# Kernel tuning notes

Hardware: AMD Instinct MI355X
Metric: run time of the kernel (lower is better)

## Reference

```python
import jax, jax.numpy as jnp
import numpy as np

LAYERS = 2
HEADS = 4
TYPE_IDX = 1  # type='logic' -> 1
HIDDEN = 256
HEAD_DIM = HIDDEN // HEADS
EPS = 1e-6


def setup_inputs() -> dict:
    key = jax.random.key(0)
    ks = jax.random.split(key, 12)
    B, S, H = 4, 2048, HIDDEN
    inputs = jax.random.normal(ks[0], (B, S, H), jnp.float32)
    graphs = jax.random.uniform(ks[1], (B, 2, S, S), jnp.float32)
    biases_batch = jax.random.normal(ks[2], (B, 2, S, S), jnp.float32)
    s_h = 1.0 / np.sqrt(H).astype(np.float32)
    s_d = 1.0 / np.sqrt(HEAD_DIM).astype(np.float32)
    gc_w = jax.random.normal(ks[3], (LAYERS, H, H), jnp.float32) * s_h
    gc_b = jnp.zeros((LAYERS, H), jnp.float32)
    attn_w = jax.random.normal(ks[4], (LAYERS, HEAD_DIM, H), jnp.float32) * s_h  # conv1 (1x1) weight
    attn_a = jax.random.normal(ks[5], (LAYERS, HEAD_DIM), jnp.float32) * s_d     # conv2_1 (1x1) weight
    ln_a = jnp.ones((H,), jnp.float32)
    ln_b = jnp.zeros((H,), jnp.float32)
    w1 = jax.random.normal(ks[6], (H, H), jnp.float32) * s_h
    w1b = jnp.zeros((H,), jnp.float32)
    w2 = jax.random.normal(ks[7], (H, H), jnp.float32) * s_h
    w2b = jnp.zeros((H,), jnp.float32)
    return dict(inputs=inputs, graphs=graphs, biases_batch=biases_batch,
                gc_w=gc_w, gc_b=gc_b, attn_w=attn_w, attn_a=attn_a,
                ln_a=ln_a, ln_b=ln_b, w1=w1, w1b=w1b, w2=w2, w2b=w2b)


def reference(inputs, graphs, biases_batch, gc_w, gc_b, attn_w, attn_a, ln_a, ln_b, w1, w1b, w2, w2b):
    adj = graphs[:, TYPE_IDX]          # [b,s,s]
    bias = biases_batch[:, TYPE_IDX]   # [b,s,s]
    x0 = inputs
    x = inputs
    for i in range(LAYERS):
        # GraphConvolution: adj @ (x @ W) + b
        mf = jnp.einsum('bij,bjh->bih', adj, x @ gc_w[i]) + gc_b[i]
        # Node_Attn_head (NOTE: original uses conv2_1 for BOTH f_1 and f_2)
        seq_fts = jnp.einsum('bsh,dh->bsd', mf, attn_w[i])      # [b,s,d]
        f = seq_fts @ attn_a[i]                                  # [b,s]
        logits = jax.nn.leaky_relu(f[:, :, None] + f[:, None, :])  # f_2^T + f_1 -> [b,s,s]
        coefs = jax.nn.softmax(logits + bias, axis=1)            # Softmax(dim=1)
        ret = jax.nn.leaky_relu(jnp.einsum('bij,bjd->bid', coefs, seq_fts))  # [b,s,d]
        # shared attention head across all HEADS -> identical outputs, concatenated
        x = jnp.tile(ret, (1, 1, HEADS)) + x
    # LayerNorm (torch.std is unbiased -> ddof=1), residual to original inputs
    mean = x.mean(-1, keepdims=True)
    std = jnp.std(x, axis=-1, keepdims=True, ddof=1)
    g = ln_a * (x - mean) / (std + EPS) + ln_b + x0
    # PositionwiseFeedForward (dropout inactive in eval)
    ff = jax.nn.relu(g @ w1.T + w1b) @ w2.T + w2b
    return ff + g
```

## Files before the change

kernel.cpp:

```cpp
#include <hip/hip_runtime.h>
#include <math.h>

#define BB 4
#define SS 2048
#define HH 256
#define DD 64
#define NLAYERS 2
#define NPART 128

#define XSC  (1.f/64.f)
#define XSCI 64.f
#define FSC  (1.f/256.f)
#define WSC  256.f
#define LNWSC 5.5451774444795624f

typedef _Float16 f16;
typedef f16 half8 __attribute__((ext_vector_type(8)));
typedef f16 half4 __attribute__((ext_vector_type(4)));
typedef float f32x4 __attribute__((ext_vector_type(4)));
#define MFMA16(a, b, c) __builtin_amdgcn_mfma_f32_16x16x32_f16(a, b, c, 0, 0, 0)

__device__ __forceinline__ float lrelu(float v) { return v > 0.f ? v : 0.01f * v; }
__device__ __forceinline__ int enc(float f) { int i = __float_as_int(f); return i >= 0 ? i : (i ^ 0x7fffffff); }
__device__ __forceinline__ float dec(int k) { int i = k >= 0 ? k : (k ^ 0x7fffffff); return __int_as_float(i); }
__device__ __forceinline__ void split8(const float* v, half8& h, half8& l) {
    #pragma unroll
    for (int e = 0; e < 8; ++e) {
        f16 hh = (f16)v[e]; h[e] = hh; l[e] = (f16)((v[e] - (float)hh) * 2048.f);
    }
}

__global__ __launch_bounds__(256) void split_scale(
    const float* __restrict__ src, f16* __restrict__ dh, f16* __restrict__ dl, float scale)
{
    long i = ((long)blockIdx.x * 256 + threadIdx.x) * 8;
    float4 a = *(const float4*)&src[i];
    float4 b = *(const float4*)&src[i + 4];
    float v[8] = {a.x * scale, a.y * scale, a.z * scale, a.w * scale,
                  b.x * scale, b.y * scale, b.z * scale, b.w * scale};
    half8 h, l; split8(v, h, l);
    *(half8*)&dh[i] = h; *(half8*)&dl[i] = l;
}

__global__ __launch_bounds__(256) void prep_wy(
    const float* __restrict__ gc_w, const float* __restrict__ gc_b,
    const float* __restrict__ attn_w,
    f16* __restrict__ WysH, f16* __restrict__ WysL, float* __restrict__ by,
    const float* __restrict__ w1, const float* __restrict__ w2,
    f16* __restrict__ w1h, f16* __restrict__ w1l,
    f16* __restrict__ w2h, f16* __restrict__ w2l, int* __restrict__ FMXi)
{
    int L = blockIdx.x >> 6, d = blockIdx.x & 63;
    int h = threadIdx.x;
    const float* gwr = gc_w + (long)L * HH * HH + (long)h * HH;
    const float* aw = attn_w + (long)L * DD * HH + (long)d * HH;
    float acc = 0.f;
    #pragma unroll 4
    for (int hp = 0; hp < HH; hp += 4) {
        float4 g4 = *(const float4*)&gwr[hp];
        float4 a4 = *(const float4*)&aw[hp];
        acc += g4.x * a4.x + g4.y * a4.y + g4.z * a4.z + g4.w * a4.w;
    }
    f16 hh = (f16)acc;
    WysH[((long)L * DD + d) * HH + h] = hh;
    WysL[((long)L * DD + d) * HH + h] = (f16)((acc - (float)hh) * 2048.f);
    if (h == 0) {
        float ba = 0.f;
        const float* gb = gc_b + (long)L * HH;
        for (int hp = 0; hp < HH; ++hp) ba += gb[hp] * aw[hp];
        by[L * DD + d] = ba;
    }
    int gt = blockIdx.x * 256 + h;
    #pragma unroll
    for (int p = 0; p < 4; ++p) {
        int e = gt * 4 + p;
        if (e < 65536) {
            float v = w1[e]; f16 x = (f16)v;
            w1h[e] = x; w1l[e] = (f16)((v - (float)x) * 2048.f);
        } else {
            int e2 = e - 65536;
            float v = w2[e2]; f16 x = (f16)v;
            w2h[e2] = x; w2l[e2] = (f16)((v - (float)x) * 2048.f);
        }
    }
    if (blockIdx.x == 0 && h < 2 * BB) FMXi[h] = enc(-1e30f);
}

__global__ __launch_bounds__(256) void y_mfma(
    const f16* __restrict__ xh, const f16* __restrict__ xl,
    const f16* __restrict__ WyhL, const f16* __restrict__ WylL,
    f16* __restrict__ yTh, f16* __restrict__ yTl)
{
    const int tid = threadIdx.x;
    const int w = tid >> 6, l = tid & 63;
    const int gw = blockIdx.x * 4 + w;
    const int b = gw >> 7, st = gw & 127;
    const int s0 = st * 16;
    const int lr = l & 15, kg = (l >> 4) * 8;
    const f16* Aph = xh + ((long)b * SS + s0 + lr) * HH;
    const f16* Apl = xl + ((long)b * SS + s0 + lr) * HH;
    f32x4 acch[4] = {}, accm[4] = {};
    #pragma unroll
    for (int k0 = 0; k0 < HH; k0 += 32) {
        half8 ah = *(const half8*)(Aph + k0 + kg);
        half8 al = *(const half8*)(Apl + k0 + kg);
        #pragma unroll
        for (int dt = 0; dt < 4; ++dt) {
            long boff = (long)(dt * 16 + lr) * HH + k0 + kg;
            half8 bh = *(const half8*)(WyhL + boff);
            half8 bl = *(const half8*)(WylL + boff);
            acch[dt] = MFMA16(ah, bh, acch[dt]);
            accm[dt] = MFMA16(ah, bl, accm[dt]);
            accm[dt] = MFMA16(al, bh, accm[dt]);
        }
    }
    const int rg0 = (l >> 4) * 4;
    #pragma unroll
    for (int dt = 0; dt < 4; ++dt) {
        int d = dt * 16 + lr;
        half4 h4, l4;
        #pragma unroll
        for (int rr = 0; rr < 4; ++rr) {
            float v = acch[dt][rr] + accm[dt][rr] * (1.f / 2048.f);
            f16 hh = (f16)v; h4[rr] = hh; l4[rr] = (f16)((v - (float)hh) * 2048.f);
        }
        long ob = ((long)b * DD + d) * SS + s0 + rg0;
        *(half4*)(yTh + ob) = h4;
        *(half4*)(yTl + ob) = l4;
    }
}

__global__ __launch_bounds__(512, 2) void ftp_fused(
    const float* __restrict__ adjB,
    const f16* __restrict__ yTh, const f16* __restrict__ yTl,
    const float* __restrict__ byL, const float* __restrict__ aaL,
    float* __restrict__ F, f16* __restrict__ fTh, f16* __restrict__ fTl,
    int* __restrict__ fmxSlot)
{
    __shared__ float Ls[8][16][68];
    __shared__ float fmaxS[16];
    const int b = blockIdx.y;
    const int i0 = blockIdx.x * 16;
    const int tid = threadIdx.x;
    const int w = tid >> 6, l = tid & 63, lr = l & 15, kg = (l >> 4) * 8;
    const float* Arow = adjB + (long)b * 2 * SS * SS + (long)(i0 + lr) * SS;
    const f16* Bh = yTh + ((long)b * DD + lr) * SS;
    const f16* Bl = yTl + ((long)b * DD + lr) * SS;

    f32x4 acch[4] = {}, accm[4] = {};
    #pragma unroll
    for (int ks = 0; ks < 256; ks += 32) {
        int k = w * 256 + ks + kg;
        float4 a0 = *(const float4*)(Arow + k);
        float4 a1 = *(const float4*)(Arow + k + 4);
        float av[8] = {a0.x, a0.y, a0.z, a0.w, a1.x, a1.y, a1.z, a1.w};
        half8 ah, al; split8(av, ah, al);
        #pragma unroll
        for (int dt = 0; dt < 4; ++dt) {
            long off = (long)dt * 16 * SS + k;
            half8 bh = *(const half8*)(Bh + off);
            half8 bl = *(const half8*)(Bl + off);
            acch[dt] = MFMA16(ah, bh, acch[dt]);
            accm[dt] = MFMA16(ah, bl, accm[dt]);
            accm[dt] = MFMA16(al, bh, accm[dt]);
        }
    }
    const int rg0 = (l >> 4) * 4;
    #pragma unroll
    for (int dt = 0; dt < 4; ++dt)
        #pragma unroll
        for (int rr = 0; rr < 4; ++rr)
            Ls[w][rg0 + rr][dt * 16 + lr] = acch[dt][rr] + accm[dt][rr] * (1.f / 2048.f);
    __syncthreads();

    {
        int r = tid >> 5, q = tid & 31, c0 = q * 2;
        float s0 = 0.f, s1 = 0.f;
        #pragma unroll
        for (int ww = 0; ww < 8; ++ww) { s0 += Ls[ww][r][c0]; s1 += Ls[ww][r][c0 + 1]; }
        s0 = s0 * XSCI + byL[c0];
        s1 = s1 * XSCI + byL[c0 + 1];
        Ls[0][r][c0] = s0; Ls[0][r][c0 + 1] = s1;
        float dot = s0 * aaL[c0] + s1 * aaL[c0 + 1];
        dot += __shfl_xor(dot, 1, 64);
        dot += __shfl_xor(dot, 2, 64);
        dot += __shfl_xor(dot, 4, 64);
        dot += __shfl_xor(dot, 8, 64);
        dot += __shfl_xor(dot, 16, 64);
        if (q == 0) { F[b * SS + i0 + r] = dot; fmaxS[r] = dot; }
    }
    __syncthreads();
    if (tid == 0) {
        float m = -1e30f;
        #pragma unroll
        for (int r = 0; r < 16; ++r) m = fmaxf(m, fmaxS[r]);
        atomicMax(fmxSlot + b, enc(m));
    }
    if (tid < 256) {
        int d = tid >> 2, sq = (tid & 3) * 4;
        half4 h4, l4;
        #pragma unroll
        for (int e = 0; e < 4; ++e) {
            float v = Ls[0][sq + e][d] * FSC;
            f16 hh = (f16)v; h4[e] = hh; l4[e] = (f16)((v - (float)hh) * 2048.f);
        }
        long ob = ((long)b * DD + d) * SS + i0 + sq;
        *(half4*)(fTh + ob) = h4;
        *(half4*)(fTl + ob) = l4;
    }
}

__global__ __launch_bounds__(512) void col_stats_part(
    const float* __restrict__ biasb, const float* __restrict__ f,
    const int* __restrict__ fmxSlot,
    float* __restrict__ partS, float* __restrict__ Mv)
{
    __shared__ float fs[32];
    const int b = blockIdx.z;
    const int chunk = blockIdx.y;
    const int half = threadIdx.x >> 8;
    const int t = threadIdx.x & 255;
    const int j0 = blockIdx.x * 1024 + t * 4;
    const float* bb = biasb + (long)b * 2 * SS * SS;
    const int ibase = chunk * 32 + half * 16;

    if (threadIdx.x < 32) fs[threadIdx.x] = f[b * SS + chunk * 32 + threadIdx.x];

    float fj[4], M[4], s[4] = {0.f, 0.f, 0.f, 0.f};
    const float fmx = dec(fmxSlot[b]);
    #pragma unroll
    for (int q = 0; q < 4; ++q) {
        fj[q] = f[b * SS + j0 + q];
        M[q] = lrelu(fmx + fj[q]) + 8.f;
    }
    __syncthreads();

    #pragma unroll
    for (int ii = 0; ii < 16; ii += 2) {
        float fi0 = fs[half * 16 + ii], fi1 = fs[half * 16 + ii + 1];
        float4 b0 = *(const float4*)&bb[(long)(ibase + ii) * SS + j0];
        float4 b1 = *(const float4*)&bb[(long)(ibase + ii + 1) * SS + j0];
        s[0] += __expf(lrelu(fi0 + fj[0]) + b0.x - M[0]);
        s[1] += __expf(lrelu(fi0 + fj[1]) + b0.y - M[1]);
        s[2] += __expf(lrelu(fi0 + fj[2]) + b0.z - M[2]);
        s[3] += __expf(lrelu(fi0 + fj[3]) + b0.w - M[3]);
        s[0] += __expf(lrelu(fi1 + fj[0]) + b1.x - M[0]);
        s[1] += __expf(lrelu(fi1 + fj[1]) + b1.y - M[1]);
        s[2] += __expf(lrelu(fi1 + fj[2]) + b1.z - M[2]);
        s[3] += __expf(lrelu(fi1 + fj[3]) + b1.w - M[3]);
    }
    const int c = chunk * 2 + half;
    #pragma unroll
    for (int q = 0; q < 4; ++q)
        partS[((long)c * BB + b) * SS + j0 + q] = s[q];
    if (chunk == 0 && half == 0) {
        #pragma unroll
        for (int q = 0; q < 4; ++q) Mv[b * SS + j0 + q] = M[q];
    }
}

__global__ __launch_bounds__(256) void col_stats_merge(
    const float* __restrict__ partS, const float* __restrict__ Mv,
    float* __restrict__ Cv)
{
    __shared__ float red[4][64];
    const int b = blockIdx.y;
    const int jl = threadIdx.x & 63;
    const int p = threadIdx.x >> 6;
    const int j = blockIdx.x * 64 + jl;
    float s = 0.f;
    #pragma unroll
    for (int k = 0; k < 32; ++k)
        s += partS[((long)(p * 32 + k) * BB + b) * SS + j];
    red[p][jl] = s;
    __syncthreads();
    if (p == 0) {
        float tot = ((red[0][jl] + red[1][jl]) + (red[2][jl] + red[3][jl]));
        Cv[b * SS + j] = LNWSC - __logf(tot) - Mv[b * SS + j];
    }
}

__global__ __launch_bounds__(512, 2) void pvp_fused(
    const float* __restrict__ biasb, const float* __restrict__ f,
    const float* __restrict__ Cv,
    const f16* __restrict__ fTh, const f16* __restrict__ fTl,
    const float* __restrict__ xin, float* __restrict__ X,
    f16* __restrict__ xh, f16* __restrict__ xl, int writeSplit)
{
    __shared__ float Ls[8][16][68];
    const int b = blockIdx.y;
    const int i0 = blockIdx.x * 16;
    const int tid = threadIdx.x;
    const int w = tid >> 6, l = tid & 63, lr = l & 15, kg = (l >> 4) * 8;
    const int irow = i0 + lr;
    const float fi = f[b * SS + irow];
    const float* brow = biasb + (long)b * 2 * SS * SS + (long)irow * SS;
    const float* fb = f + b * SS;
    const float* cb = Cv + b * SS;
    const f16* Bh = fTh + ((long)b * DD + lr) * SS;
    const f16* Bl = fTl + ((long)b * DD + lr) * SS;

    f32x4 acch[4] = {}, accm[4] = {};
    #pragma unroll
    for (int jc = 0; jc < 256; jc += 32) {
        const int jb = w * 256 + jc + kg;
        float4 bs0 = *(const float4*)(brow + jb);
        float4 bs1 = *(const float4*)(brow + jb + 4);
        float4 fj0 = *(const float4*)(fb + jb);
        float4 fj1 = *(const float4*)(fb + jb + 4);
        float4 cj0 = *(const float4*)(cb + jb);
        float4 cj1 = *(const float4*)(cb + jb + 4);
        float wv[8];
        wv[0] = __expf(lrelu(fi + fj0.x) + bs0.x + cj0.x);
        wv[1] = __expf(lrelu(fi + fj0.y) + bs0.y + cj0.y);
        wv[2] = __expf(lrelu(fi + fj0.z) + bs0.z + cj0.z);
        wv[3] = __expf(lrelu(fi + fj0.w) + bs0.w + cj0.w);
        wv[4] = __expf(lrelu(fi + fj1.x) + bs1.x + cj1.x);
        wv[5] = __expf(lrelu(fi + fj1.y) + bs1.y + cj1.y);
        wv[6] = __expf(lrelu(fi + fj1.z) + bs1.z + cj1.z);
        wv[7] = __expf(lrelu(fi + fj1.w) + bs1.w + cj1.w);
        half8 ah, al; split8(wv, ah, al);
        #pragma unroll
        for (int dt = 0; dt < 4; ++dt) {
            long off = (long)dt * 16 * SS + jb;
            half8 bh = *(const half8*)(Bh + off);
            half8 bl = *(const half8*)(Bl + off);
            acch[dt] = MFMA16(ah, bh, acch[dt]);
            accm[dt] = MFMA16(ah, bl, accm[dt]);
            accm[dt] = MFMA16(al, bh, accm[dt]);
        }
    }
    const int rg0 = (l >> 4) * 4;
    #pragma unroll
    for (int dt = 0; dt < 4; ++dt)
        #pragma unroll
        for (int rr = 0; rr < 4; ++rr)
            Ls[w][rg0 + rr][dt * 16 + lr] = acch[dt][rr] + accm[dt][rr] * (1.f / 2048.f);
    __syncthreads();

    {
        int r = tid >> 5, q = tid & 31, dq = q * 2;
        float v0 = 0.f, v1 = 0.f;
        #pragma unroll
        for (int ww = 0; ww < 8; ++ww) { v0 += Ls[ww][r][dq]; v1 += Ls[ww][r][dq + 1]; }
        v0 = lrelu(v0); v1 = lrelu(v1);
        long rowoff = ((long)b * SS + i0 + r) * HH;
        #pragma unroll
        for (int rep = 0; rep < 4; ++rep) {
            long off = rowoff + rep * DD + dq;
            float o0 = v0 + xin[off];
            float o1 = v1 + xin[off + 1];
            X[off] = o0; X[off + 1] = o1;
            if (writeSplit) {
                float s0 = o0 * XSC, s1 = o1 * XSC;
                f16 h0 = (f16)s0, h1 = (f16)s1;
                xh[off] = h0; xl[off] = (f16)((s0 - (float)h0) * 2048.f);
                xh[off + 1] = h1; xl[off + 1] = (f16)((s1 - (float)h1) * 2048.f);
            }
        }
    }
}

__global__ __launch_bounds__(256) void layernorm_g(
    const float* __restrict__ x, const float* __restrict__ x0,
    const float* __restrict__ lna, const float* __restrict__ lnb,
    float* __restrict__ g, f16* __restrict__ gh, f16* __restrict__ gl)
{
    const int wave = threadIdx.x >> 6, lane = threadIdx.x & 63;
    const long row = (long)blockIdx.x * 4 + wave;
    const int c0 = lane * 4;
    float4 v = *(const float4*)&x[row * HH + c0];
    float s = v.x + v.y + v.z + v.w;
    #pragma unroll
    for (int off = 32; off; off >>= 1) s += __shfl_xor(s, off, 64);
    float mean = s * (1.f / HH);
    float dx = v.x - mean, dy = v.y - mean, dz = v.z - mean, dw = v.w - mean;
    float sq = dx * dx + dy * dy + dz * dz + dw * dw;
    #pragma unroll
    for (int off = 32; off; off >>= 1) sq += __shfl_xor(sq, off, 64);
    float stdv = sqrtf(sq * (1.f / (HH - 1)));
    float rinv = 1.f / (stdv + 1e-6f);
    float4 la = *(const float4*)&lna[c0];
    float4 lb = *(const float4*)&lnb[c0];
    float4 xo = *(const float4*)&x0[row * HH + c0];
    float gv[4];
    gv[0] = la.x * dx * rinv + lb.x + xo.x;
    gv[1] = la.y * dy * rinv + lb.y + xo.y;
    gv[2] = la.z * dz * rinv + lb.z + xo.z;
    gv[3] = la.w * dw * rinv + lb.w + xo.w;
    *(float4*)&g[row * HH + c0] = *(float4*)gv;
    half4 h4, l4;
    #pragma unroll
    for (int e = 0; e < 4; ++e) {
        f16 hh = (f16)gv[e]; h4[e] = hh; l4[e] = (f16)((gv[e] - (float)hh) * 2048.f);
    }
    *(half4*)&gh[row * HH + c0] = h4;
    *(half4*)&gl[row * HH + c0] = l4;
}

__global__ __launch_bounds__(256) void ffn_mfma(
    const f16* __restrict__ Ah, const f16* __restrict__ Al,
    const f16* __restrict__ Bh, const f16* __restrict__ Bl,
    const float* __restrict__ bias, const float* __restrict__ res,
    float* __restrict__ outF, f16* __restrict__ outH, f16* __restrict__ outL,
    int doRelu)
{
    __shared__ float Ls[64][68];
    const int i0 = blockIdx.x * 64, j0 = blockIdx.y * 64;
    const int tid = threadIdx.x;
    const int w = tid >> 6, l = tid & 63, lr = l & 15, kg = (l >> 4) * 8;
    const f16* Aph = Ah + ((long)i0 + w * 16 + lr) * HH;
    const f16* Apl = Al + ((long)i0 + w * 16 + lr) * HH;
    f32x4 acch[4] = {}, accm[4] = {};
    #pragma unroll
    for (int k0 = 0; k0 < HH; k0 += 32) {
        half8 ah = *(const half8*)(Aph + k0 + kg);
        half8 al = *(const half8*)(Apl + k0 + kg);
        #pragma unroll
        for (int dt = 0; dt < 4; ++dt) {
            long boff = ((long)(j0 + dt * 16 + lr)) * HH + k0 + kg;
            half8 bh = *(const half8*)(Bh + boff);
            half8 bl = *(const half8*)(Bl + boff);
            acch[dt] = MFMA16(ah, bh, acch[dt]);
            accm[dt] = MFMA16(ah, bl, accm[dt]);
            accm[dt] = MFMA16(al, bh, accm[dt]);
        }
    }
    const int rg0 = (l >> 4) * 4;
    #pragma unroll
    for (int dt = 0; dt < 4; ++dt) {
        float bj = bias[j0 + dt * 16 + lr];
        #pragma unroll
        for (int rr = 0; rr < 4; ++rr) {
            float v = acch[dt][rr] + accm[dt][rr] * (1.f / 2048.f) + bj;
            if (doRelu) v = fmaxf(v, 0.f);
            Ls[w * 16 + rg0 + rr][dt * 16 + lr] = v;
        }
    }
    __syncthreads();
    int s = tid >> 2, nq = (tid & 3) * 16;
    long go = ((long)i0 + s) * HH + j0 + nq;
    if (outF) {
        #pragma unroll
        for (int q = 0; q < 4; ++q) {
            float4 v = *(float4*)&Ls[s][nq + q * 4];
            if (res) {
                float4 r = *(const float4*)&res[go + q * 4];
                v.x += r.x; v.y += r.y; v.z += r.z; v.w += r.w;
            }
            *(float4*)&outF[go + q * 4] = v;
        }
    } else {
        float v0[8], v1[8];
        #pragma unroll
        for (int e = 0; e < 8; ++e) { v0[e] = Ls[s][nq + e]; v1[e] = Ls[s][nq + 8 + e]; }
        half8 h0, l0, h1, l1; split8(v0, h0, l0); split8(v1, h1, l1);
        *(half8*)&outH[go] = h0; *(half8*)&outH[go + 8] = h1;
        *(half8*)&outL[go] = l0; *(half8*)&outL[go + 8] = l1;
    }
}

extern "C" void kernel_launch(void* const* d_in, const int* in_sizes, int n_in,
                              void* d_out, int out_size, void* d_ws, size_t ws_size,
                              hipStream_t stream)
{
    const float* inputs = (const float*)d_in[0];
    const float* graphs = (const float*)d_in[1];
    const float* biases = (const float*)d_in[2];
    const float* gc_w   = (const float*)d_in[3];
    const float* gc_b   = (const float*)d_in[4];
    const float* attn_w = (const float*)d_in[5];
    const float* attn_a = (const float*)d_in[6];
    const float* ln_a   = (const float*)d_in[7];
    const float* ln_b   = (const float*)d_in[8];
    const float* w1     = (const float*)d_in[9];
    const float* w1b    = (const float*)d_in[10];
    const float* w2     = (const float*)d_in[11];
    const float* w2b    = (const float*)d_in[12];
    float* out = (float*)d_out;

    float* ws   = (float*)d_ws;
    float* X    = ws;
    float* G    = ws + 2097152;
    float* PTS  = ws + 4194304;
    float* F    = ws + 5242880;
    float* Mv   = ws + 5251072;
    float* Cv   = ws + 5259264;
    float* by   = ws + 5267456;
    int*   FMXi = (int*)(ws + 5267584);
    f16* WysH   = (f16*)(ws + 5267712);
    f16* WysL   = (f16*)(ws + 5284096);
    f16* yTh    = (f16*)(ws + 5300480);
    f16* yTl    = (f16*)(ws + 5562624);
    f16* fTh    = (f16*)(ws + 5824768);
    f16* fTl    = (f16*)(ws + 6086912);
    f16* xh     = (f16*)(ws + 6349056);
    f16* xl     = (f16*)(ws + 7397632);
    f16* gh     = (f16*)(ws + 8446208);
    f16* gl     = (f16*)(ws + 9494784);
    f16* h1h    = (f16*)(ws + 10543360);
    f16* h1l    = (f16*)(ws + 11591936);
    f16* w1h    = (f16*)(ws + 12640512);
    f16* w1l    = (f16*)(ws + 12673280);
    f16* w2h    = (f16*)(ws + 12706048);
    f16* w2l    = (f16*)(ws + 12738816);

    const float* adjBase  = graphs + (long)SS * SS;
    const float* biasBase = biases + (long)SS * SS;

    prep_wy<<<128, 256, 0, stream>>>(gc_w, gc_b, attn_w, WysH, WysL, by,
                                     w1, w2, w1h, w1l, w2h, w2l, FMXi);
    split_scale<<<1024, 256, 0, stream>>>(inputs, xh, xl, XSC);

    for (int L = 0; L < NLAYERS; ++L) {
        y_mfma<<<128, 256, 0, stream>>>(xh, xl,
            WysH + (long)L * DD * HH, WysL + (long)L * DD * HH, yTh, yTl);
        ftp_fused<<<dim3(128, BB), 512, 0, stream>>>(
            adjBase, yTh, yTl, by + L * DD, attn_a + (long)L * DD,
            F, fTh, fTl, FMXi + L * BB);
        col_stats_part<<<dim3(2, 64, BB), 512, 0, stream>>>(
            biasBase, F, FMXi + L * BB, PTS, Mv);
        col_stats_merge<<<dim3(32, BB), 256, 0, stream>>>(PTS, Mv, Cv);
        pvp_fused<<<dim3(128, BB), 512, 0, stream>>>(
            biasBase, F, Cv, fTh, fTl,
            (L == 0) ? inputs : X, X, xh, xl, (L == 0) ? 1 : 0);
    }

    layernorm_g<<<2048, 256, 0, stream>>>(X, inputs, ln_a, ln_b, G, gh, gl);
    ffn_mfma<<<dim3(128, 4), 256, 0, stream>>>(gh, gl, w1h, w1l, w1b,
                                               nullptr, nullptr, h1h, h1l, 1);
    ffn_mfma<<<dim3(128, 4), 256, 0, stream>>>(h1h, h1l, w2h, w2l, w2b,
                                               G, out, nullptr, nullptr, 0);
}
```

Measured before the change: 303.8 us.

## Cache layer-2 softmax exponentials as fp16 and merge prep kernels

In layer 2, col_stats_part now writes the computed exponentials, scaled and cast to fp16, into a B×S×S buffer. A new pvp_fused2 reads these cached values and a per-column reciprocal-sum scale instead of re-reading the fp32 bias matrix and recomputing exp. This replaces the second fp32 bias read and exp pass in the attention-value product with a half-size fp16 read, but it adds a 32MB write in the column-stats kernel and some precision risk from fp16-stored weights. Separately, split_scale is folded into the weight-prep kernel as extra blocks, which removes one launch.

```diff
diff --git a/kernel.cpp b/kernel.cpp
--- a/kernel.cpp
+++ b/kernel.cpp
@@ -13,6 +13,8 @@
 #define FSC  (1.f/256.f)
 #define WSC  256.f
 #define LNWSC 5.5451774444795624f
+#define EC1  190781.31f
+#define CWC  1.3418535e-3f
 
 typedef _Float16 f16;
 typedef f16 half8 __attribute__((ext_vector_type(8)));
@@ -30,26 +32,25 @@
     }
 }
 
-__global__ __launch_bounds__(256) void split_scale(
-    const float* __restrict__ src, f16* __restrict__ dh, f16* __restrict__ dl, float scale)
-{
-    long i = ((long)blockIdx.x * 256 + threadIdx.x) * 8;
-    float4 a = *(const float4*)&src[i];
-    float4 b = *(const float4*)&src[i + 4];
-    float v[8] = {a.x * scale, a.y * scale, a.z * scale, a.w * scale,
-                  b.x * scale, b.y * scale, b.z * scale, b.w * scale};
-    half8 h, l; split8(v, h, l);
-    *(half8*)&dh[i] = h; *(half8*)&dl[i] = l;
-}
-
-__global__ __launch_bounds__(256) void prep_wy(
+__global__ __launch_bounds__(256) void prep_all(
     const float* __restrict__ gc_w, const float* __restrict__ gc_b,
     const float* __restrict__ attn_w,
     f16* __restrict__ WysH, f16* __restrict__ WysL, float* __restrict__ by,
     const float* __restrict__ w1, const float* __restrict__ w2,
     f16* __restrict__ w1h, f16* __restrict__ w1l,
-    f16* __restrict__ w2h, f16* __restrict__ w2l, int* __restrict__ FMXi)
-{
+    f16* __restrict__ w2h, f16* __restrict__ w2l, int* __restrict__ FMXi,
+    const float* __restrict__ inputs, f16* __restrict__ xh, f16* __restrict__ xl)
+{
+    if (blockIdx.x >= 128) {
+        long i = ((long)(blockIdx.x - 128) * 256 + threadIdx.x) * 8;
+        float4 a = *(const float4*)&inputs[i];
+        float4 b = *(const float4*)&inputs[i + 4];
+        float v[8] = {a.x * XSC, a.y * XSC, a.z * XSC, a.w * XSC,
+                      b.x * XSC, b.y * XSC, b.z * XSC, b.w * XSC};
+        half8 h, l; split8(v, h, l);
+        *(half8*)&xh[i] = h; *(half8*)&xl[i] = l;
+        return;
+    }
     int L = blockIdx.x >> 6, d = blockIdx.x & 63;
     int h = threadIdx.x;
     const float* gwr = gc_w + (long)L * HH * HH + (long)h * HH;
@@ -213,7 +214,7 @@
 __global__ __launch_bounds__(512) void col_stats_part(
     const float* __restrict__ biasb, const float* __restrict__ f,
     const int* __restrict__ fmxSlot,
-    float* __restrict__ partS, float* __restrict__ Mv)
+    float* __restrict__ partS, float* __restrict__ Mv, f16* __restrict__ EhL)
 {
     __shared__ float fs[32];
     const int b = blockIdx.z;
@@ -240,20 +241,31 @@
         float fi0 = fs[half * 16 + ii], fi1 = fs[half * 16 + ii + 1];
         float4 b0 = *(const float4*)&bb[(long)(ibase + ii) * SS + j0];
         float4 b1 = *(const float4*)&bb[(long)(ibase + ii + 1) * SS + j0];
-        s[0] += __expf(lrelu(fi0 + fj[0]) + b0.x - M[0]);
-        s[1] += __expf(lrelu(fi0 + fj[1]) + b0.y - M[1]);
-        s[2] += __expf(lrelu(fi0 + fj[2]) + b0.z - M[2]);
-        s[3] += __expf(lrelu(fi0 + fj[3]) + b0.w - M[3]);
-        s[0] += __expf(lrelu(fi1 + fj[0]) + b1.x - M[0]);
-        s[1] += __expf(lrelu(fi1 + fj[1]) + b1.y - M[1]);
-        s[2] += __expf(lrelu(fi1 + fj[2]) + b1.z - M[2]);
-        s[3] += __expf(lrelu(fi1 + fj[3]) + b1.w - M[3]);
+        float e00 = __expf(lrelu(fi0 + fj[0]) + b0.x - M[0]);
+        float e01 = __expf(lrelu(fi0 + fj[1]) + b0.y - M[1]);
+        float e02 = __expf(lrelu(fi0 + fj[2]) + b0.z - M[2]);
+        float e03 = __expf(lrelu(fi0 + fj[3]) + b0.w - M[3]);
+        float e10 = __expf(lrelu(fi1 + fj[0]) + b1.x - M[0]);
+        float e11 = __expf(lrelu(fi1 + fj[1]) + b1.y - M[1]);
+        float e12 = __expf(lrelu(fi1 + fj[2]) + b1.z - M[2]);
+        float e13 = __expf(lrelu(fi1 + fj[3]) + b1.w - M[3]);
+        s[0] += e00 + e10; s[1] += e01 + e11;
+        s[2] += e02 + e12; s[3] += e03 + e13;
+        if (EhL) {
+            half4 h0, h1;
+            h0[0] = (f16)(e00 * EC1); h0[1] = (f16)(e01 * EC1);
+            h0[2] = (f16)(e02 * EC1); h0[3] = (f16)(e03 * EC1);
+            h1[0] = (f16)(e10 * EC1); h1[1] = (f16)(e11 * EC1);
+            h1[2] = (f16)(e12 * EC1); h1[3] = (f16)(e13 * EC1);
+            *(half4*)&EhL[((long)b * SS + ibase + ii) * SS + j0] = h0;
+            *(half4*)&EhL[((long)b * SS + ibase + ii + 1) * SS + j0] = h1;
+        }
     }
     const int c = chunk * 2 + half;
     #pragma unroll
     for (int q = 0; q < 4; ++q)
         partS[((long)c * BB + b) * SS + j0 + q] = s[q];
-    if (chunk == 0 && half == 0) {
+    if (c == 0) {
         #pragma unroll
         for (int q = 0; q < 4; ++q) Mv[b * SS + j0 + q] = M[q];
     }
@@ -261,7 +273,7 @@
 
 __global__ __launch_bounds__(256) void col_stats_merge(
     const float* __restrict__ partS, const float* __restrict__ Mv,
-    float* __restrict__ Cv)
+    float* __restrict__ Cv, float* __restrict__ Cw)
 {
     __shared__ float red[4][64];
     const int b = blockIdx.y;
@@ -277,6 +289,7 @@
     if (p == 0) {
         float tot = ((red[0][jl] + red[1][jl]) + (red[2][jl] + red[3][jl]));
         Cv[b * SS + j] = LNWSC - __logf(tot) - Mv[b * SS + j];
+        Cw[b * SS + j] = CWC / tot;
     }
 }
 
@@ -285,7 +298,7 @@
     const float* __restrict__ Cv,
     const f16* __restrict__ fTh, const f16* __restrict__ fTl,
     const float* __restrict__ xin, float* __restrict__ X,
-    f16* __restrict__ xh, f16* __restrict__ xl, int writeSplit)
+    f16* __restrict__ xh, f16* __restrict__ xl)
 {
     __shared__ float Ls[8][16][68];
     const int b = blockIdx.y;
@@ -351,12 +364,73 @@
             float o0 = v0 + xin[off];
             float o1 = v1 + xin[off + 1];
             X[off] = o0; X[off + 1] = o1;
-            if (writeSplit) {
-                float s0 = o0 * XSC, s1 = o1 * XSC;
-                f16 h0 = (f16)s0, h1 = (f16)s1;
-                xh[off] = h0; xl[off] = (f16)((s0 - (float)h0) * 2048.f);
-                xh[off + 1] = h1; xl[off + 1] = (f16)((s1 - (float)h1) * 2048.f);
-            }
+            float s0 = o0 * XSC, s1 = o1 * XSC;
+            f16 h0 = (f16)s0, h1 = (f16)s1;
+            xh[off] = h0; xl[off] = (f16)((s0 - (float)h0) * 2048.f);
+            xh[off + 1] = h1; xl[off + 1] = (f16)((s1 - (float)h1) * 2048.f);
+        }
+    }
+}
+
+__global__ __launch_bounds__(512, 2) void pvp_fused2(
+    const f16* __restrict__ Eh, const float* __restrict__ Cw,
+    const f16* __restrict__ fTh, const f16* __restrict__ fTl,
+    const float* __restrict__ xin, float* __restrict__ X)
+{
+    __shared__ float Ls[8][16][68];
+    const int b = blockIdx.y;
+    const int i0 = blockIdx.x * 16;
+    const int tid = threadIdx.x;
+    const int w = tid >> 6, l = tid & 63, lr = l & 15, kg = (l >> 4) * 8;
+    const int irow = i0 + lr;
+    const f16* Erow = Eh + ((long)b * SS + irow) * SS;
+    const float* cw = Cw + (long)b * SS;
+    const f16* Bh = fTh + ((long)b * DD + lr) * SS;
+    const f16* Bl = fTl + ((long)b * DD + lr) * SS;
+
+    f32x4 acch[4] = {}, accm[4] = {};
+    #pragma unroll
+    for (int jc = 0; jc < 256; jc += 32) {
+        const int jb = w * 256 + jc + kg;
+        half8 ev = *(const half8*)(Erow + jb);
+        float4 c0 = *(const float4*)(cw + jb);
+        float4 c1 = *(const float4*)(cw + jb + 4);
+        float wv[8];
+        wv[0] = (float)ev[0] * c0.x; wv[1] = (float)ev[1] * c0.y;
+        wv[2] = (float)ev[2] * c0.z; wv[3] = (float)ev[3] * c0.w;
+        wv[4] = (float)ev[4] * c1.x; wv[5] = (float)ev[5] * c1.y;
+        wv[6] = (float)ev[6] * c1.z; wv[7] = (float)ev[7] * c1.w;
+        half8 ah, al; split8(wv, ah, al);
+        #pragma unroll
+        for (int dt = 0; dt < 4; ++dt) {
+            long off = (long)dt * 16 * SS + jb;
+            half8 bh = *(const half8*)(Bh + off);
+            half8 bl = *(const half8*)(Bl + off);
+            acch[dt] = MFMA16(ah, bh, acch[dt]);
+            accm[dt] = MFMA16(ah, bl, accm[dt]);
+            accm[dt] = MFMA16(al, bh, accm[dt]);
+        }
+    }
+    const int rg0 = (l >> 4) * 4;
+    #pragma unroll
+    for (int dt = 0; dt < 4; ++dt)
+        #pragma unroll
+        for (int rr = 0; rr < 4; ++rr)
+            Ls[w][rg0 + rr][dt * 16 + lr] = acch[dt][rr] + accm[dt][rr] * (1.f / 2048.f);
+    __syncthreads();
+
+    {
+        int r = tid >> 5, q = tid & 31, dq = q * 2;
+        float v0 = 0.f, v1 = 0.f;
+        #pragma unroll
+        for (int ww = 0; ww < 8; ++ww) { v0 += Ls[ww][r][dq]; v1 += Ls[ww][r][dq + 1]; }
+        v0 = lrelu(v0); v1 = lrelu(v1);
+        long rowoff = ((long)b * SS + i0 + r) * HH;
+        #pragma unroll
+        for (int rep = 0; rep < 4; ++rep) {
+            long off = rowoff + rep * DD + dq;
+            X[off] = v0 + xin[off];
+            X[off + 1] = v1 + xin[off + 1];
         }
     }
 }
@@ -486,31 +560,33 @@
     float* F    = ws + 5242880;
     float* Mv   = ws + 5251072;
     float* Cv   = ws + 5259264;
-    float* by   = ws + 5267456;
-    int*   FMXi = (int*)(ws + 5267584);
-    f16* WysH   = (f16*)(ws + 5267712);
-    f16* WysL   = (f16*)(ws + 5284096);
-    f16* yTh    = (f16*)(ws + 5300480);
-    f16* yTl    = (f16*)(ws + 5562624);
-    f16* fTh    = (f16*)(ws + 5824768);
-    f16* fTl    = (f16*)(ws + 6086912);
-    f16* xh     = (f16*)(ws + 6349056);
-    f16* xl     = (f16*)(ws + 7397632);
-    f16* gh     = (f16*)(ws + 8446208);
-    f16* gl     = (f16*)(ws + 9494784);
-    f16* h1h    = (f16*)(ws + 10543360);
-    f16* h1l    = (f16*)(ws + 11591936);
-    f16* w1h    = (f16*)(ws + 12640512);
-    f16* w1l    = (f16*)(ws + 12673280);
-    f16* w2h    = (f16*)(ws + 12706048);
-    f16* w2l    = (f16*)(ws + 12738816);
+    float* Cw   = ws + 5267456;
+    float* by   = ws + 5275648;
+    int*   FMXi = (int*)(ws + 5275776);
+    f16* WysH   = (f16*)(ws + 5275904);
+    f16* WysL   = (f16*)(ws + 5292288);
+    f16* yTh    = (f16*)(ws + 5308672);
+    f16* yTl    = (f16*)(ws + 5570816);
+    f16* fTh    = (f16*)(ws + 5832960);
+    f16* fTl    = (f16*)(ws + 6095104);
+    f16* xh     = (f16*)(ws + 6357248);
+    f16* xl     = (f16*)(ws + 7405824);
+    f16* gh     = (f16*)(ws + 8454400);
+    f16* gl     = (f16*)(ws + 9502976);
+    f16* h1h    = (f16*)(ws + 10551552);
+    f16* h1l    = (f16*)(ws + 11600128);
+    f16* w1h    = (f16*)(ws + 12648704);
+    f16* w1l    = (f16*)(ws + 12681472);
+    f16* w2h    = (f16*)(ws + 12714240);
+    f16* w2l    = (f16*)(ws + 12747008);
+    f16* Eh     = (f16*)(ws + 12779776);
 
     const float* adjBase  = graphs + (long)SS * SS;
     const float* biasBase = biases + (long)SS * SS;
 
-    prep_wy<<<128, 256, 0, stream>>>(gc_w, gc_b, attn_w, WysH, WysL, by,
-                                     w1, w2, w1h, w1l, w2h, w2l, FMXi);
-    split_scale<<<1024, 256, 0, stream>>>(inputs, xh, xl, XSC);
+    prep_all<<<1152, 256, 0, stream>>>(gc_w, gc_b, attn_w, WysH, WysL, by,
+                                       w1, w2, w1h, w1l, w2h, w2l, FMXi,
+                                       inputs, xh, xl);
 
     for (int L = 0; L < NLAYERS; ++L) {
         y_mfma<<<128, 256, 0, stream>>>(xh, xl,
@@ -519,11 +595,15 @@
             adjBase, yTh, yTl, by + L * DD, attn_a + (long)L * DD,
             F, fTh, fTl, FMXi + L * BB);
         col_stats_part<<<dim3(2, 64, BB), 512, 0, stream>>>(
-            biasBase, F, FMXi + L * BB, PTS, Mv);
-        col_stats_merge<<<dim3(32, BB), 256, 0, stream>>>(PTS, Mv, Cv);
-        pvp_fused<<<dim3(128, BB), 512, 0, stream>>>(
-            biasBase, F, Cv, fTh, fTl,
-            (L == 0) ? inputs : X, X, xh, xl, (L == 0) ? 1 : 0);
+            biasBase, F, FMXi + L * BB, PTS, Mv, (L == 1) ? Eh : (f16*)nullptr);
+        col_stats_merge<<<dim3(32, BB), 256, 0, stream>>>(PTS, Mv, Cv, Cw);
+        if (L == 0) {
+            pvp_fused<<<dim3(128, BB), 512, 0, stream>>>(
+                biasBase, F, Cv, fTh, fTl, inputs, X, xh, xl);
+        } else {
+            pvp_fused2<<<dim3(128, BB), 512, 0, stream>>>(
+                Eh, Cw, fTh, fTl, X, X);
+        }
     }
 
     layernorm_g<<<2048, 256, 0, stream>>>(X, inputs, ln_a, ln_b, G, gh, gl);
```

Result: no change. 298.6 us (-1.7%).
